# Kernel tuning notes

Measured on AMD Instinct MI355X. Metric: run time of the kernel, lower is better.

## Reference

```python
import jax, jax.numpy as jnp
import numpy as np

N = 4096
CIN = 128
COUT = 128
J = 2
SLOPE = 0.2        # LeakyReLU negative slope (GAT-style)
NEG = -9.0e15      # mask fill value from the source
ATT = J * COUT     # att_slice


def _leaky(v):
    return jnp.where(v >= 0, v, SLOPE * v)


def setup_inputs() -> dict:
    key = jax.random.key(0)
    ks = jax.random.split(key, 12)
    x = jax.random.normal(ks[0], (N, CIN), dtype=jnp.float32)

    def sparse_op(k):
        kv, km = jax.random.split(k)
        vals = jax.random.normal(kv, (N, N), dtype=jnp.float32)
        mask = jax.random.uniform(km, (N, N)) < 0.05
        return jnp.where(mask, vals, 0.0)

    Lu = sparse_op(ks[1])
    Ld = sparse_op(ks[2])
    P = jax.random.normal(ks[3], (N, N), dtype=jnp.float32) * 0.01  # harmonic projector

    s = 1.0 / np.sqrt(CIN)
    Wi_w = jax.random.uniform(ks[4], (J, CIN, COUT), minval=-s, maxval=s)
    Wi_b = jax.random.uniform(ks[5], (J, COUT), minval=-s, maxval=s)
    Ws_w = jax.random.uniform(ks[6], (J, CIN, COUT), minval=-s, maxval=s)
    Ws_b = jax.random.uniform(ks[7], (J, COUT), minval=-s, maxval=s)
    Wh_w = jax.random.uniform(ks[8], (CIN, COUT), minval=-s, maxval=s)
    Wh_b = jax.random.uniform(ks[9], (COUT,), minval=-s, maxval=s)
    att_irr = jax.random.normal(ks[10], (2 * ATT, 1), dtype=jnp.float32) * 0.1
    att_sol = jax.random.normal(ks[11], (2 * ATT, 1), dtype=jnp.float32) * 0.1
    return {"x": x, "Lu": Lu, "Ld": Ld, "P": P,
            "Wi_w": Wi_w, "Wi_b": Wi_b, "Ws_w": Ws_w, "Ws_b": Ws_b,
            "Wh_w": Wh_w, "Wh_b": Wh_b, "att_irr": att_irr, "att_sol": att_sol}


def reference(x, Lu, Ld, P, Wi_w, Wi_b, Ws_w, Ws_b, Wh_w, Wh_b, att_irr, att_sol):
    n = x.shape[0]
    # concat_j W_irr[j](x) -> [N, J*COUT] (j-major matches torch.cat along dim=1)
    x_irr = (jnp.einsum('nc,jco->njo', x, Wi_w) + Wi_b[None]).reshape(n, ATT)
    x_sol = (jnp.einsum('nc,jco->njo', x, Ws_w) + Ws_b[None]).reshape(n, ATT)

    # GAT-style scores: E[i,j] = leaky(s1[i] + s2[j])
    E_irr = _leaky(x_irr @ att_irr[:ATT] + (x_irr @ att_irr[ATT:]).T)
    E_sol = _leaky(x_sol @ att_sol[:ATT] + (x_sol @ att_sol[ATT:]).T)
    E_irr = jnp.where(Ld != 0, E_irr, NEG)
    E_sol = jnp.where(Lu != 0, E_sol, NEG)
    alpha_irr = jax.nn.softmax(E_irr, axis=1)  # dropout: eval mode -> identity
    alpha_sol = jax.nn.softmax(E_sol, axis=1)

    z = (alpha_irr @ x) @ Wi_w[0] + Wi_b[0] + (alpha_sol @ x) @ Ws_w[0] + Ws_b[0]
    for p in range(1, J):  # Laplacian-power aggregation
        alpha_irr = alpha_irr @ Ld
        alpha_sol = alpha_sol @ Lu
        z = z + (alpha_irr @ x) @ Wi_w[p] + Wi_b[p]
        z = z + (alpha_sol @ x) @ Ws_w[p] + Ws_b[p]
    z = z + (P @ x) @ Wh_w + Wh_b
    return z
```

## Files before the change

kernel.cpp:

```cpp
#include <hip/hip_runtime.h>

#define NN 4096
#define IDX_CAP 512
#define SEG_CAP 160
#define SLOPE 0.2f

typedef float f4_t __attribute__((ext_vector_type(4)));

#define V_OFF     0
#define C_OFF     512
#define BT_OFF    516
#define S_OFF     1024
#define HXI_OFF   32768
#define HXS_OFF   (HXI_OFF + NN*128)
#define UI_OFF    (HXS_OFF + NN*128)
#define US_OFF    (UI_OFF + NN*128)
#define XWH_OFF   (US_OFF + NN*128)
#define OI_OFF    (XWH_OFF + NN*128)
#define OS_OFF    (OI_OFF + NN*128)
#define ZP_OFF    (OS_OFF + NN*128)
#define WS_FLOATS (ZP_OFF + 8*NN*128)
#define IDX_BYTE_OFF ((size_t)WS_FLOATS * 4)
#define CNT_BYTE_OFF (IDX_BYTE_OFF + (size_t)2*NN*IDX_CAP*2)

__global__ __launch_bounds__(128) void k_prep(
    const float* __restrict__ Wi_w, const float* __restrict__ Wi_b,
    const float* __restrict__ Ws_w, const float* __restrict__ Ws_b,
    const float* __restrict__ Wh_b, const float* __restrict__ att_irr,
    const float* __restrict__ att_sol, float* __restrict__ ws) {
  const int t = threadIdx.x;
  float v1i = 0.f, v2i = 0.f, v1s = 0.f, v2s = 0.f;
  for (int j = 0; j < 2; ++j) {
    for (int o = 0; o < 128; ++o) {
      const float wi = Wi_w[j*16384 + t*128 + o];
      const float wv = Ws_w[j*16384 + t*128 + o];
      v1i += wi * att_irr[j*128 + o];
      v2i += wi * att_irr[256 + j*128 + o];
      v1s += wv * att_sol[j*128 + o];
      v2s += wv * att_sol[256 + j*128 + o];
    }
  }
  ws[V_OFF + t]       = v1i;
  ws[V_OFF + 128 + t] = v2i;
  ws[V_OFF + 256 + t] = v1s;
  ws[V_OFF + 384 + t] = v2s;
  ws[BT_OFF + t] = Wi_b[t] + Wi_b[128 + t] + Ws_b[t] + Ws_b[128 + t] + Wh_b[t];
  if (t < 4) {
    const float* bb = (t < 2) ? Wi_b : Ws_b;
    const float* aa = ((t < 2) ? att_irr : att_sol) + ((t & 1) ? 256 : 0);
    float c = 0.f;
    for (int k = 0; k < 256; ++k) c += bb[k] * aa[k];
    ws[C_OFF + t] = c;
  }
}

__global__ __launch_bounds__(256) void k_scores(const float* __restrict__ x,
                                                float* __restrict__ ws) {
  const int wave = threadIdx.x >> 6, lane = threadIdx.x & 63;
  const int row = blockIdx.x * 4 + wave;
  const float* v = ws + V_OFF;
  const float x0 = x[row*128 + lane];
  const float x1 = x[row*128 + 64 + lane];
  float p0 = x0 * v[lane]       + x1 * v[64 + lane];
  float p1 = x0 * v[128 + lane] + x1 * v[192 + lane];
  float p2 = x0 * v[256 + lane] + x1 * v[320 + lane];
  float p3 = x0 * v[384 + lane] + x1 * v[448 + lane];
  #pragma unroll
  for (int off = 32; off; off >>= 1) {
    p0 += __shfl_down(p0, off);
    p1 += __shfl_down(p1, off);
    p2 += __shfl_down(p2, off);
    p3 += __shfl_down(p3, off);
  }
  if (lane == 0) {
    ws[S_OFF + row]          = p0 + ws[C_OFF + 0];
    ws[S_OFF + NN + row]     = p1 + ws[C_OFF + 1];
    ws[S_OFF + 2*NN + row]   = p2 + ws[C_OFF + 2];
    ws[S_OFF + 3*NN + row]   = p3 + ws[C_OFF + 3];
  }
}

__global__ __launch_bounds__(256) void k_spmm_emit(
    const float* __restrict__ Ld, const float* __restrict__ Lu,
    const float* __restrict__ x, float* __restrict__ ws,
    unsigned short* __restrict__ idxbuf, int* __restrict__ cntbuf) {
  const int row = blockIdx.x & (NN - 1);
  const int br  = blockIdx.x >> 12;
  const float* __restrict__ Lrow = (br ? Lu : Ld) + (size_t)row * NN;
  float* __restrict__ Hx = ws + (br ? HXS_OFF : HXI_OFF);
  unsigned short* __restrict__ idxg = idxbuf + (size_t)(br*NN + row) * IDX_CAP;
  const float2* __restrict__ x2 = (const float2*)x;
  const int t = threadIdx.x;
  const int w = t >> 6, lane = t & 63;
  const unsigned long long lmask = (1ull << lane) - 1ull;

  __shared__ short jseg[4][SEG_CAP];
  __shared__ float vseg[4][SEG_CAP];
  __shared__ int   wcnt[4];
  __shared__ int   off[5];
  __shared__ short jl[IDX_CAP];
  __shared__ float vl[IDX_CAP];
  __shared__ float red[4][128];

  const f4_t* __restrict__ Lrow4 = (const f4_t*)Lrow;
  f4_t lv[4];
  #pragma unroll
  for (int i = 0; i < 4; ++i) lv[i] = __builtin_nontemporal_load(&Lrow4[i*256 + t]);

  int base = 0;
  #pragma unroll
  for (int i = 0; i < 4; ++i) {
    #pragma unroll
    for (int c = 0; c < 4; ++c) {
      const float v = lv[i][c];
      const unsigned long long bm = __ballot(v != 0.f);
      if (v != 0.f) {
        const int pos = base + (int)__popcll(bm & lmask);
        if (pos < SEG_CAP) {
          jseg[w][pos] = (short)((i*256 + t)*4 + c);
          vseg[w][pos] = v;
        }
      }
      base += (int)__popcll(bm);
    }
  }
  if (lane == 0) wcnt[w] = base;
  __syncthreads();
  if (t == 0) {
    int o = 0, ov = 0;
    #pragma unroll
    for (int s = 0; s < 4; ++s) { off[s] = o; ov |= (wcnt[s] > SEG_CAP); o += wcnt[s]; }
    off[4] = (ov || o > IDX_CAP) ? (IDX_CAP + 1) : o;
    cntbuf[br*NN + row] = off[4];
  }
  __syncthreads();
  const int m = off[4];

  if (m <= IDX_CAP) {
    const int o = off[w], c = wcnt[w];
    for (int k = lane; k < c; k += 64) {
      const short j = jseg[w][k];
      jl[o + k] = j;
      vl[o + k] = vseg[w][k];
      idxg[o + k] = (unsigned short)j;
    }
  }
  __syncthreads();

  float acc0 = 0.f, acc1 = 0.f;
  if (m <= IDX_CAP) {
    int p = w;
    for (; p + 28 < m; p += 32) {
      const int j0 = jl[p],    j1 = jl[p+4],  j2 = jl[p+8],  j3 = jl[p+12];
      const int j4 = jl[p+16], j5 = jl[p+20], j6 = jl[p+24], j7 = jl[p+28];
      const float v0 = vl[p],    v1 = vl[p+4],  v2 = vl[p+8],  v3 = vl[p+12];
      const float v4 = vl[p+16], v5 = vl[p+20], v6 = vl[p+24], v7 = vl[p+28];
      const float2 g0 = x2[j0*64 + lane];
      const float2 g1 = x2[j1*64 + lane];
      const float2 g2 = x2[j2*64 + lane];
      const float2 g3 = x2[j3*64 + lane];
      const float2 g4 = x2[j4*64 + lane];
      const float2 g5 = x2[j5*64 + lane];
      const float2 g6 = x2[j6*64 + lane];
      const float2 g7 = x2[j7*64 + lane];
      acc0 += v0*g0.x; acc1 += v0*g0.y;
      acc0 += v1*g1.x; acc1 += v1*g1.y;
      acc0 += v2*g2.x; acc1 += v2*g2.y;
      acc0 += v3*g3.x; acc1 += v3*g3.y;
      acc0 += v4*g4.x; acc1 += v4*g4.y;
      acc0 += v5*g5.x; acc1 += v5*g5.y;
      acc0 += v6*g6.x; acc1 += v6*g6.y;
      acc0 += v7*g7.x; acc1 += v7*g7.y;
    }
    for (; p < m; p += 4) {
      const int j = jl[p]; const float v = vl[p];
      const float2 g = x2[j*64 + lane];
      acc0 += v*g.x; acc1 += v*g.y;
    }
  } else {
    for (int j = w*1024; j < (w+1)*1024; ++j) {
      const float v = Lrow[j];
      if (v != 0.f) {
        const float2 g = x2[j*64 + lane];
        acc0 += v*g.x; acc1 += v*g.y;
      }
    }
  }
  red[w][lane*2]     = acc0;
  red[w][lane*2 + 1] = acc1;
  __syncthreads();
  if (t < 128)
    Hx[row*128 + t] = red[0][t] + red[1][t] + red[2][t] + red[3][t];
}

__global__ __launch_bounds__(256) void k_ugemm(
    const float* __restrict__ x, const float* __restrict__ Wi_w,
    const float* __restrict__ Ws_w, const float* __restrict__ Wh_w,
    float* __restrict__ ws) {
  const int rb = blockIdx.x;
  const int sel = blockIdx.y;
  const float* A[2]; const float* W[2]; int npass; float* out;
  if (sel == 0)      { A[0]=x; W[0]=Wi_w; A[1]=ws+HXI_OFF; W[1]=Wi_w+16384; npass=2; out=ws+UI_OFF; }
  else if (sel == 1) { A[0]=x; W[0]=Ws_w; A[1]=ws+HXS_OFF; W[1]=Ws_w+16384; npass=2; out=ws+US_OFF; }
  else               { A[0]=x; W[0]=Wh_w; A[1]=nullptr;    W[1]=nullptr;    npass=1; out=ws+XWH_OFF; }

  __shared__ __align__(16) float At[32][33];
  __shared__ __align__(16) float Wt[32][132];
  const int t = threadIdx.x;
  const int rg = t >> 4, cg = t & 15;
  const int r0 = rb * 32;
  float acc[2][8];
  #pragma unroll
  for (int i = 0; i < 2; ++i)
    #pragma unroll
    for (int j = 0; j < 8; ++j) acc[i][j] = 0.f;

  for (int ps = 0; ps < npass; ++ps) {
    const float* __restrict__ Ap = A[ps];
    const float* __restrict__ Wp = W[ps];
    for (int k0 = 0; k0 < 128; k0 += 32) {
      __syncthreads();
      {
        const int row = t >> 3, kq = t & 7;
        const float4 av = *(const float4*)&Ap[(r0 + row)*128 + k0 + kq*4];
        At[row][kq*4+0] = av.x; At[row][kq*4+1] = av.y;
        At[row][kq*4+2] = av.z; At[row][kq*4+3] = av.w;
      }
      #pragma unroll
      for (int l = 0; l < 4; ++l) {
        const int idx = t + l*256;
        const int kr = idx >> 5, c4 = idx & 31;
        const float4 wv = *(const float4*)&Wp[(k0 + kr)*128 + c4*4];
        Wt[kr][c4*4+0] = wv.x; Wt[kr][c4*4+1] = wv.y;
        Wt[kr][c4*4+2] = wv.z; Wt[kr][c4*4+3] = wv.w;
      }
      __syncthreads();
      #pragma unroll
      for (int k = 0; k < 32; ++k) {
        const float a0 = At[rg*2 + 0][k];
        const float a1 = At[rg*2 + 1][k];
        const float4 b0 = *(const float4*)&Wt[k][cg*8];
        const float4 b1 = *(const float4*)&Wt[k][cg*8 + 4];
        acc[0][0] += a0*b0.x; acc[0][1] += a0*b0.y; acc[0][2] += a0*b0.z; acc[0][3] += a0*b0.w;
        acc[0][4] += a0*b1.x; acc[0][5] += a0*b1.y; acc[0][6] += a0*b1.z; acc[0][7] += a0*b1.w;
        acc[1][0] += a1*b0.x; acc[1][1] += a1*b0.y; acc[1][2] += a1*b0.z; acc[1][3] += a1*b0.w;
        acc[1][4] += a1*b1.x; acc[1][5] += a1*b1.y; acc[1][6] += a1*b1.z; acc[1][7] += a1*b1.w;
      }
    }
  }
  #pragma unroll
  for (int i = 0; i < 2; ++i) {
    const int r = r0 + rg*2 + i;
    #pragma unroll
    for (int j = 0; j < 8; ++j) out[r*128 + cg*8 + j] = acc[i][j];
  }
}

__global__ __launch_bounds__(256) void k_pgemm(const float* __restrict__ P,
                                               const float* __restrict__ ws,
                                               float* __restrict__ zpart) {
  const int rbl = blockIdx.x;
  const int kz  = blockIdx.y;
  const float* __restrict__ Xw = ws + XWH_OFF;

  __shared__ __align__(16) float Pt[64][33];
  __shared__ __align__(16) float Xt[32][132];
  const int t = threadIdx.x;
  const int rg = t >> 4, cg = t & 15;
  const int r0 = rbl * 64;
  const int kbase = kz * 512;
  float acc[4][8];
  #pragma unroll
  for (int i = 0; i < 4; ++i)
    #pragma unroll
    for (int j = 0; j < 8; ++j) acc[i][j] = 0.f;

  for (int k0 = kbase; k0 < kbase + 512; k0 += 32) {
    __syncthreads();
    #pragma unroll
    for (int l = 0; l < 2; ++l) {
      const int idx = t + l*256;
      const int row = idx >> 3, kq = idx & 7;
      const float4 pv = *(const float4*)&P[(size_t)(r0 + row)*NN + k0 + kq*4];
      Pt[row][kq*4+0] = pv.x; Pt[row][kq*4+1] = pv.y;
      Pt[row][kq*4+2] = pv.z; Pt[row][kq*4+3] = pv.w;
    }
    #pragma unroll
    for (int l = 0; l < 4; ++l) {
      const int idx = t + l*256;
      const int kr = idx >> 5, c4 = idx & 31;
      const float4 xv = *(const float4*)&Xw[(k0 + kr)*128 + c4*4];
      Xt[kr][c4*4+0] = xv.x; Xt[kr][c4*4+1] = xv.y;
      Xt[kr][c4*4+2] = xv.z; Xt[kr][c4*4+3] = xv.w;
    }
    __syncthreads();
    #pragma unroll
    for (int k = 0; k < 32; ++k) {
      const float a0 = Pt[rg*4 + 0][k];
      const float a1 = Pt[rg*4 + 1][k];
      const float a2 = Pt[rg*4 + 2][k];
      const float a3 = Pt[rg*4 + 3][k];
      const float4 b0 = *(const float4*)&Xt[k][cg*8];
      const float4 b1 = *(const float4*)&Xt[k][cg*8 + 4];
      acc[0][0] += a0*b0.x; acc[0][1] += a0*b0.y; acc[0][2] += a0*b0.z; acc[0][3] += a0*b0.w;
      acc[0][4] += a0*b1.x; acc[0][5] += a0*b1.y; acc[0][6] += a0*b1.z; acc[0][7] += a0*b1.w;
      acc[1][0] += a1*b0.x; acc[1][1] += a1*b0.y; acc[1][2] += a1*b0.z; acc[1][3] += a1*b0.w;
      acc[1][4] += a1*b1.x; acc[1][5] += a1*b1.y; acc[1][6] += a1*b1.z; acc[1][7] += a1*b1.w;
      acc[2][0] += a2*b0.x; acc[2][1] += a2*b0.y; acc[2][2] += a2*b0.z; acc[2][3] += a2*b0.w;
      acc[2][4] += a2*b1.x; acc[2][5] += a2*b1.y; acc[2][6] += a2*b1.z; acc[2][7] += a2*b1.w;
      acc[3][0] += a3*b0.x; acc[3][1] += a3*b0.y; acc[3][2] += a3*b0.z; acc[3][3] += a3*b0.w;
      acc[3][4] += a3*b1.x; acc[3][5] += a3*b1.y; acc[3][6] += a3*b1.z; acc[3][7] += a3*b1.w;
    }
  }
  float* __restrict__ zp = zpart + (size_t)kz * NN * 128;
  #pragma unroll
  for (int i = 0; i < 4; ++i) {
    const int r = r0 + rg*4 + i;
    #pragma unroll
    for (int j = 0; j < 8; ++j) zp[r*128 + cg*8 + j] = acc[i][j];
  }
}

__global__ __launch_bounds__(256) void k_attn(
    const float* __restrict__ Ld, const float* __restrict__ Lu,
    float* __restrict__ ws, const unsigned short* __restrict__ idxbuf,
    const int* __restrict__ cntbuf) {
  const int row = blockIdx.x & (NN - 1);
  const int br  = blockIdx.x >> 12;
  const float* __restrict__ U = ws + (br ? US_OFF : UI_OFF);
  const float2* __restrict__ U2 = (const float2*)U;
  float* __restrict__ O = ws + (br ? OS_OFF : OI_OFF);
  const float s1 = ws[S_OFF + (br ? 2*NN : 0) + row];
  const float* __restrict__ s2a = ws + S_OFF + (br ? 3*NN : NN);
  const int cnt = cntbuf[br*NN + row];
  const int t = threadIdx.x;
  const int w = t >> 6, lane = t & 63;

  __shared__ int   jl[IDX_CAP];
  __shared__ float el[IDX_CAP];
  __shared__ float red[4][128];
  __shared__ float rsum[256];
  __shared__ float dsh[4];

  float acc0 = 0.f, acc1 = 0.f;
  if (cnt > 0 && cnt <= IDX_CAP) {
    const unsigned short* __restrict__ idx = idxbuf + (size_t)(br*NN + row) * IDX_CAP;
    float dpart = 0.f;
    for (int p = t; p < cnt; p += 256) {
      const int j = idx[p];
      const float sc = s1 + s2a[j];
      const float e = expf(sc >= 0.f ? sc : SLOPE * sc);
      jl[p] = j; el[p] = e; dpart += e;
    }
    rsum[t] = dpart;
    __syncthreads();
    if (t < 128) rsum[t] += rsum[t + 128];
    __syncthreads();
    if (t < 64) {
      float v = rsum[t] + rsum[t + 64];
      #pragma unroll
      for (int off = 32; off; off >>= 1) v += __shfl_down(v, off);
      if (t == 0) dsh[0] = v;
    }
    __syncthreads();
    const float den = dsh[0];
    int p = w;
    for (; p + 28 < cnt; p += 32) {
      const int j0 = jl[p],    j1 = jl[p+4],  j2 = jl[p+8],  j3 = jl[p+12];
      const int j4 = jl[p+16], j5 = jl[p+20], j6 = jl[p+24], j7 = jl[p+28];
      const float e0 = el[p],    e1 = el[p+4],  e2 = el[p+8],  e3 = el[p+12];
      const float e4 = el[p+16], e5 = el[p+20], e6 = el[p+24], e7 = el[p+28];
      const float2 g0 = U2[j0*64 + lane];
      const float2 g1 = U2[j1*64 + lane];
      const float2 g2 = U2[j2*64 + lane];
      const float2 g3 = U2[j3*64 + lane];
      const float2 g4 = U2[j4*64 + lane];
      const float2 g5 = U2[j5*64 + lane];
      const float2 g6 = U2[j6*64 + lane];
      const float2 g7 = U2[j7*64 + lane];
      acc0 += e0*g0.x; acc1 += e0*g0.y;
      acc0 += e1*g1.x; acc1 += e1*g1.y;
      acc0 += e2*g2.x; acc1 += e2*g2.y;
      acc0 += e3*g3.x; acc1 += e3*g3.y;
      acc0 += e4*g4.x; acc1 += e4*g4.y;
      acc0 += e5*g5.x; acc1 += e5*g5.y;
      acc0 += e6*g6.x; acc1 += e6*g6.y;
      acc0 += e7*g7.x; acc1 += e7*g7.y;
    }
    for (; p < cnt; p += 4) {
      const int j = jl[p]; const float e = el[p];
      const float2 g = U2[j*64 + lane];
      acc0 += e*g.x; acc1 += e*g.y;
    }
    red[w][lane*2]     = acc0;
    red[w][lane*2 + 1] = acc1;
    __syncthreads();
    if (t < 128)
      O[row*128 + t] = (red[0][t] + red[1][t] + red[2][t] + red[3][t]) / den;
  } else if (cnt == 0) {
    for (int j = w*1024; j < (w+1)*1024; ++j) {
      const float2 g = U2[j*64 + lane];
      acc0 += g.x; acc1 += g.y;
    }
    red[w][lane*2]     = acc0;
    red[w][lane*2 + 1] = acc1;
    __syncthreads();
    if (t < 128)
      O[row*128 + t] = (red[0][t] + red[1][t] + red[2][t] + red[3][t]) * (1.f / NN);
  } else {
    const float* __restrict__ Lrow = (br ? Lu : Ld) + (size_t)row * NN;
    float dp = 0.f;
    for (int j = w*1024; j < (w+1)*1024; ++j) {
      const float v = Lrow[j];
      if (v != 0.f) {
        const float sc = s1 + s2a[j];
        const float e = expf(sc >= 0.f ? sc : SLOPE * sc);
        const float2 g = U2[j*64 + lane];
        acc0 += e*g.x; acc1 += e*g.y;
        dp += e;
      }
    }
    if (lane == 0) dsh[w] = dp;
    red[w][lane*2]     = acc0;
    red[w][lane*2 + 1] = acc1;
    __syncthreads();
    const float den = dsh[0] + dsh[1] + dsh[2] + dsh[3];
    if (t < 128)
      O[row*128 + t] = (red[0][t] + red[1][t] + red[2][t] + red[3][t]) / den;
  }
}

__global__ __launch_bounds__(256) void k_combine(const float* __restrict__ ws,
                                                 float* __restrict__ z) {
  const int i = blockIdx.x * 256 + threadIdx.x;
  const int col = i & 127;
  float acc = ws[BT_OFF + col] + ws[OI_OFF + i] + ws[OS_OFF + i];
  #pragma unroll
  for (int kz = 0; kz < 8; ++kz) acc += ws[ZP_OFF + kz*NN*128 + i];
  z[i] = acc;
}

extern "C" void kernel_launch(void* const* d_in, const int* in_sizes, int n_in,
                              void* d_out, int out_size, void* d_ws, size_t ws_size,
                              hipStream_t stream) {
  const float* x       = (const float*)d_in[0];
  const float* Lu      = (const float*)d_in[1];
  const float* Ld      = (const float*)d_in[2];
  const float* P       = (const float*)d_in[3];
  const float* Wi_w    = (const float*)d_in[4];
  const float* Wi_b    = (const float*)d_in[5];
  const float* Ws_w    = (const float*)d_in[6];
  const float* Ws_b    = (const float*)d_in[7];
  const float* Wh_w    = (const float*)d_in[8];
  const float* Wh_b    = (const float*)d_in[9];
  const float* att_irr = (const float*)d_in[10];
  const float* att_sol = (const float*)d_in[11];
  float* z  = (float*)d_out;
  float* ws = (float*)d_ws;
  unsigned short* idxbuf = (unsigned short*)((char*)d_ws + IDX_BYTE_OFF);
  int*            cntbuf = (int*)((char*)d_ws + CNT_BYTE_OFF);

  k_prep<<<1, 128, 0, stream>>>(Wi_w, Wi_b, Ws_w, Ws_b, Wh_b, att_irr, att_sol, ws);
  k_scores<<<1024, 256, 0, stream>>>(x, ws);
  k_spmm_emit<<<2 * NN, 256, 0, stream>>>(Ld, Lu, x, ws, idxbuf, cntbuf);
  {
    dim3 g(128, 3);
    k_ugemm<<<g, 256, 0, stream>>>(x, Wi_w, Ws_w, Wh_w, ws);
  }
  {
    dim3 g(64, 8);
    k_pgemm<<<g, 256, 0, stream>>>(P, ws, ws + ZP_OFF);
  }
  k_attn<<<2 * NN, 256, 0, stream>>>(Ld, Lu, ws, idxbuf, cntbuf);
  k_combine<<<NN * 128 / 256, 256, 0, stream>>>(ws, z);
}
```

Before: 399.0 us.

## Restructure gathers to float4, swizzle LDS tiles, split pgemm columns, interleave branch rows

The x@Wh GEMM moves into a merged pre-pass kernel alongside the score computation. The sparse gather loops in spmm_emit and attn now use 16-byte loads, with half-waves covering alternate nonzeros and a cross-half shuffle reduction. Block-to-row mapping interleaves the Ld and Lu branches, and LDS weight tiles get a padded swizzle to avoid bank conflicts. The P GEMM is split into two column halves to double the block count, and the launch order is changed. The combined edits aim to raise gather bandwidth and occupancy, at the cost of more index arithmetic and smaller per-block tiles in pgemm.

```diff
diff --git a/kernel.cpp b/kernel.cpp
--- a/kernel.cpp
+++ b/kernel.cpp
@@ -23,6 +23,11 @@
 #define IDX_BYTE_OFF ((size_t)WS_FLOATS * 4)
 #define CNT_BYTE_OFF (IDX_BYTE_OFF + (size_t)2*NN*IDX_CAP*2)
 
+#define XI(c)   ((c) + (((c) >> 5) << 2))
+
+#define MAP_BR(bid)   (((bid) >> 2) & 1)
+#define MAP_ROW(bid)  ((((bid) >> 3) << 2) | ((bid) & 3))
+
 __global__ __launch_bounds__(128) void k_prep(
     const float* __restrict__ Wi_w, const float* __restrict__ Wi_b,
     const float* __restrict__ Ws_w, const float* __restrict__ Ws_b,
@@ -54,29 +59,80 @@
   }
 }
 
-__global__ __launch_bounds__(256) void k_scores(const float* __restrict__ x,
-                                                float* __restrict__ ws) {
-  const int wave = threadIdx.x >> 6, lane = threadIdx.x & 63;
-  const int row = blockIdx.x * 4 + wave;
-  const float* v = ws + V_OFF;
-  const float x0 = x[row*128 + lane];
-  const float x1 = x[row*128 + 64 + lane];
-  float p0 = x0 * v[lane]       + x1 * v[64 + lane];
-  float p1 = x0 * v[128 + lane] + x1 * v[192 + lane];
-  float p2 = x0 * v[256 + lane] + x1 * v[320 + lane];
-  float p3 = x0 * v[384 + lane] + x1 * v[448 + lane];
-  #pragma unroll
-  for (int off = 32; off; off >>= 1) {
-    p0 += __shfl_down(p0, off);
-    p1 += __shfl_down(p1, off);
-    p2 += __shfl_down(p2, off);
-    p3 += __shfl_down(p3, off);
-  }
-  if (lane == 0) {
-    ws[S_OFF + row]          = p0 + ws[C_OFF + 0];
-    ws[S_OFF + NN + row]     = p1 + ws[C_OFF + 1];
-    ws[S_OFF + 2*NN + row]   = p2 + ws[C_OFF + 2];
-    ws[S_OFF + 3*NN + row]   = p3 + ws[C_OFF + 3];
+__global__ __launch_bounds__(256) void k_pre2(
+    const float* __restrict__ x, const float* __restrict__ Wh_w,
+    float* __restrict__ ws) {
+  __shared__ __align__(16) float At[32][33];
+  __shared__ __align__(16) float Wt[32][144];
+  const int t = threadIdx.x;
+
+  if (blockIdx.x < 128) {
+    const int rb = blockIdx.x;
+    float* out = ws + XWH_OFF;
+    const int rg = t >> 4, cg = t & 15;
+    const int r0 = rb * 32;
+    float acc[2][8];
+    #pragma unroll
+    for (int i = 0; i < 2; ++i)
+      #pragma unroll
+      for (int j = 0; j < 8; ++j) acc[i][j] = 0.f;
+    for (int k0 = 0; k0 < 128; k0 += 32) {
+      __syncthreads();
+      {
+        const int row = t >> 3, kq = t & 7;
+        const float4 av = *(const float4*)&x[(r0 + row)*128 + k0 + kq*4];
+        At[row][kq*4+0] = av.x; At[row][kq*4+1] = av.y;
+        At[row][kq*4+2] = av.z; At[row][kq*4+3] = av.w;
+      }
+      #pragma unroll
+      for (int l = 0; l < 4; ++l) {
+        const int idx = t + l*256;
+        const int kr = idx >> 5, c4 = idx & 31;
+        const float4 wv = *(const float4*)&Wh_w[(k0 + kr)*128 + c4*4];
+        *(float4*)&Wt[kr][XI(c4*4)] = wv;
+      }
+      __syncthreads();
+      #pragma unroll
+      for (int k = 0; k < 32; ++k) {
+        const float a0 = At[rg*2 + 0][k];
+        const float a1 = At[rg*2 + 1][k];
+        const float4 b0 = *(const float4*)&Wt[k][XI(cg*8)];
+        const float4 b1 = *(const float4*)&Wt[k][XI(cg*8 + 4)];
+        acc[0][0] += a0*b0.x; acc[0][1] += a0*b0.y; acc[0][2] += a0*b0.z; acc[0][3] += a0*b0.w;
+        acc[0][4] += a0*b1.x; acc[0][5] += a0*b1.y; acc[0][6] += a0*b1.z; acc[0][7] += a0*b1.w;
+        acc[1][0] += a1*b0.x; acc[1][1] += a1*b0.y; acc[1][2] += a1*b0.z; acc[1][3] += a1*b0.w;
+        acc[1][4] += a1*b1.x; acc[1][5] += a1*b1.y; acc[1][6] += a1*b1.z; acc[1][7] += a1*b1.w;
+      }
+    }
+    #pragma unroll
+    for (int i = 0; i < 2; ++i) {
+      const int r = r0 + rg*2 + i;
+      #pragma unroll
+      for (int j = 0; j < 8; ++j) out[r*128 + cg*8 + j] = acc[i][j];
+    }
+  } else {
+    const int wave = t >> 6, lane = t & 63;
+    const int row = (blockIdx.x - 128) * 4 + wave;
+    const float* v = ws + V_OFF;
+    const float x0 = x[row*128 + lane];
+    const float x1 = x[row*128 + 64 + lane];
+    float p0 = x0 * v[lane]       + x1 * v[64 + lane];
+    float p1 = x0 * v[128 + lane] + x1 * v[192 + lane];
+    float p2 = x0 * v[256 + lane] + x1 * v[320 + lane];
+    float p3 = x0 * v[384 + lane] + x1 * v[448 + lane];
+    #pragma unroll
+    for (int off = 32; off; off >>= 1) {
+      p0 += __shfl_down(p0, off);
+      p1 += __shfl_down(p1, off);
+      p2 += __shfl_down(p2, off);
+      p3 += __shfl_down(p3, off);
+    }
+    if (lane == 0) {
+      ws[S_OFF + row]          = p0 + ws[C_OFF + 0];
+      ws[S_OFF + NN + row]     = p1 + ws[C_OFF + 1];
+      ws[S_OFF + 2*NN + row]   = p2 + ws[C_OFF + 2];
+      ws[S_OFF + 3*NN + row]   = p3 + ws[C_OFF + 3];
+    }
   }
 }
 
@@ -84,12 +140,12 @@
     const float* __restrict__ Ld, const float* __restrict__ Lu,
     const float* __restrict__ x, float* __restrict__ ws,
     unsigned short* __restrict__ idxbuf, int* __restrict__ cntbuf) {
-  const int row = blockIdx.x & (NN - 1);
-  const int br  = blockIdx.x >> 12;
+  const int bid = blockIdx.x;
+  const int br  = MAP_BR(bid);
+  const int row = MAP_ROW(bid);
   const float* __restrict__ Lrow = (br ? Lu : Ld) + (size_t)row * NN;
   float* __restrict__ Hx = ws + (br ? HXS_OFF : HXI_OFF);
   unsigned short* __restrict__ idxg = idxbuf + (size_t)(br*NN + row) * IDX_CAP;
-  const float2* __restrict__ x2 = (const float2*)x;
   const int t = threadIdx.x;
   const int w = t >> 6, lane = t & 63;
   const unsigned long long lmask = (1ull << lane) - 1ull;
@@ -147,37 +203,35 @@
   }
   __syncthreads();
 
-  float acc0 = 0.f, acc1 = 0.f;
   if (m <= IDX_CAP) {
+    const f4_t* __restrict__ x4 = (const f4_t*)x;
+    const int li = lane & 31, half = lane >> 5;
+    f4_t acc = {0.f, 0.f, 0.f, 0.f};
     int p = w;
-    for (; p + 28 < m; p += 32) {
-      const int j0 = jl[p],    j1 = jl[p+4],  j2 = jl[p+8],  j3 = jl[p+12];
-      const int j4 = jl[p+16], j5 = jl[p+20], j6 = jl[p+24], j7 = jl[p+28];
-      const float v0 = vl[p],    v1 = vl[p+4],  v2 = vl[p+8],  v3 = vl[p+12];
-      const float v4 = vl[p+16], v5 = vl[p+20], v6 = vl[p+24], v7 = vl[p+28];
-      const float2 g0 = x2[j0*64 + lane];
-      const float2 g1 = x2[j1*64 + lane];
-      const float2 g2 = x2[j2*64 + lane];
-      const float2 g3 = x2[j3*64 + lane];
-      const float2 g4 = x2[j4*64 + lane];
-      const float2 g5 = x2[j5*64 + lane];
-      const float2 g6 = x2[j6*64 + lane];
-      const float2 g7 = x2[j7*64 + lane];
-      acc0 += v0*g0.x; acc1 += v0*g0.y;
-      acc0 += v1*g1.x; acc1 += v1*g1.y;
-      acc0 += v2*g2.x; acc1 += v2*g2.y;
-      acc0 += v3*g3.x; acc1 += v3*g3.y;
-      acc0 += v4*g4.x; acc1 += v4*g4.y;
-      acc0 += v5*g5.x; acc1 += v5*g5.y;
-      acc0 += v6*g6.x; acc1 += v6*g6.y;
-      acc0 += v7*g7.x; acc1 += v7*g7.y;
-    }
-    for (; p < m; p += 4) {
-      const int j = jl[p]; const float v = vl[p];
-      const float2 g = x2[j*64 + lane];
-      acc0 += v*g.x; acc1 += v*g.y;
+    for (; 2*(p + 12) + 1 < m; p += 16) {
+      const int q0 = 2*p + half, q1 = 2*(p+4) + half,
+                q2 = 2*(p+8) + half, q3 = 2*(p+12) + half;
+      const int j0 = jl[q0], j1 = jl[q1], j2 = jl[q2], j3 = jl[q3];
+      const float v0 = vl[q0], v1 = vl[q1], v2 = vl[q2], v3 = vl[q3];
+      const f4_t g0 = x4[j0*32 + li];
+      const f4_t g1 = x4[j1*32 + li];
+      const f4_t g2 = x4[j2*32 + li];
+      const f4_t g3 = x4[j3*32 + li];
+      acc += v0*g0; acc += v1*g1; acc += v2*g2; acc += v3*g3;
+    }
+    for (; 2*p < m; p += 4) {
+      const int q = 2*p + half;
+      if (q < m) acc += vl[q] * x4[jl[q]*32 + li];
+    }
+    #pragma unroll
+    for (int c = 0; c < 4; ++c) acc[c] += __shfl_xor(acc[c], 32);
+    if (half == 0) {
+      red[w][li*4+0] = acc[0]; red[w][li*4+1] = acc[1];
+      red[w][li*4+2] = acc[2]; red[w][li*4+3] = acc[3];
     }
   } else {
+    const float2* __restrict__ x2 = (const float2*)x;
+    float acc0 = 0.f, acc1 = 0.f;
     for (int j = w*1024; j < (w+1)*1024; ++j) {
       const float v = Lrow[j];
       if (v != 0.f) {
@@ -185,9 +239,9 @@
         acc0 += v*g.x; acc1 += v*g.y;
       }
     }
-  }
-  red[w][lane*2]     = acc0;
-  red[w][lane*2 + 1] = acc1;
+    red[w][lane*2]     = acc0;
+    red[w][lane*2 + 1] = acc1;
+  }
   __syncthreads();
   if (t < 128)
     Hx[row*128 + t] = red[0][t] + red[1][t] + red[2][t] + red[3][t];
@@ -195,17 +249,15 @@
 
 __global__ __launch_bounds__(256) void k_ugemm(
     const float* __restrict__ x, const float* __restrict__ Wi_w,
-    const float* __restrict__ Ws_w, const float* __restrict__ Wh_w,
-    float* __restrict__ ws) {
+    const float* __restrict__ Ws_w, float* __restrict__ ws) {
   const int rb = blockIdx.x;
   const int sel = blockIdx.y;
-  const float* A[2]; const float* W[2]; int npass; float* out;
-  if (sel == 0)      { A[0]=x; W[0]=Wi_w; A[1]=ws+HXI_OFF; W[1]=Wi_w+16384; npass=2; out=ws+UI_OFF; }
-  else if (sel == 1) { A[0]=x; W[0]=Ws_w; A[1]=ws+HXS_OFF; W[1]=Ws_w+16384; npass=2; out=ws+US_OFF; }
-  else               { A[0]=x; W[0]=Wh_w; A[1]=nullptr;    W[1]=nullptr;    npass=1; out=ws+XWH_OFF; }
+  const float* A[2]; const float* W[2]; float* out;
+  if (sel == 0) { A[0]=x; W[0]=Wi_w; A[1]=ws+HXI_OFF; W[1]=Wi_w+16384; out=ws+UI_OFF; }
+  else          { A[0]=x; W[0]=Ws_w; A[1]=ws+HXS_OFF; W[1]=Ws_w+16384; out=ws+US_OFF; }
 
   __shared__ __align__(16) float At[32][33];
-  __shared__ __align__(16) float Wt[32][132];
+  __shared__ __align__(16) float Wt[32][144];
   const int t = threadIdx.x;
   const int rg = t >> 4, cg = t & 15;
   const int r0 = rb * 32;
@@ -215,7 +267,7 @@
     #pragma unroll
     for (int j = 0; j < 8; ++j) acc[i][j] = 0.f;
 
-  for (int ps = 0; ps < npass; ++ps) {
+  for (int ps = 0; ps < 2; ++ps) {
     const float* __restrict__ Ap = A[ps];
     const float* __restrict__ Wp = W[ps];
     for (int k0 = 0; k0 < 128; k0 += 32) {
@@ -231,16 +283,15 @@
         const int idx = t + l*256;
         const int kr = idx >> 5, c4 = idx & 31;
         const float4 wv = *(const float4*)&Wp[(k0 + kr)*128 + c4*4];
-        Wt[kr][c4*4+0] = wv.x; Wt[kr][c4*4+1] = wv.y;
-        Wt[kr][c4*4+2] = wv.z; Wt[kr][c4*4+3] = wv.w;
+        *(float4*)&Wt[kr][XI(c4*4)] = wv;
       }
       __syncthreads();
       #pragma unroll
       for (int k = 0; k < 32; ++k) {
         const float a0 = At[rg*2 + 0][k];
         const float a1 = At[rg*2 + 1][k];
-        const float4 b0 = *(const float4*)&Wt[k][cg*8];
-        const float4 b1 = *(const float4*)&Wt[k][cg*8 + 4];
+        const float4 b0 = *(const float4*)&Wt[k][XI(cg*8)];
+        const float4 b1 = *(const float4*)&Wt[k][XI(cg*8 + 4)];
         acc[0][0] += a0*b0.x; acc[0][1] += a0*b0.y; acc[0][2] += a0*b0.z; acc[0][3] += a0*b0.w;
         acc[0][4] += a0*b1.x; acc[0][5] += a0*b1.y; acc[0][6] += a0*b1.z; acc[0][7] += a0*b1.w;
         acc[1][0] += a1*b0.x; acc[1][1] += a1*b0.y; acc[1][2] += a1*b0.z; acc[1][3] += a1*b0.w;
@@ -256,79 +307,14 @@
   }
 }
 
-__global__ __launch_bounds__(256) void k_pgemm(const float* __restrict__ P,
-                                               const float* __restrict__ ws,
-                                               float* __restrict__ zpart) {
-  const int rbl = blockIdx.x;
-  const int kz  = blockIdx.y;
-  const float* __restrict__ Xw = ws + XWH_OFF;
-
-  __shared__ __align__(16) float Pt[64][33];
-  __shared__ __align__(16) float Xt[32][132];
-  const int t = threadIdx.x;
-  const int rg = t >> 4, cg = t & 15;
-  const int r0 = rbl * 64;
-  const int kbase = kz * 512;
-  float acc[4][8];
-  #pragma unroll
-  for (int i = 0; i < 4; ++i)
-    #pragma unroll
-    for (int j = 0; j < 8; ++j) acc[i][j] = 0.f;
-
-  for (int k0 = kbase; k0 < kbase + 512; k0 += 32) {
-    __syncthreads();
-    #pragma unroll
-    for (int l = 0; l < 2; ++l) {
-      const int idx = t + l*256;
-      const int row = idx >> 3, kq = idx & 7;
-      const float4 pv = *(const float4*)&P[(size_t)(r0 + row)*NN + k0 + kq*4];
-      Pt[row][kq*4+0] = pv.x; Pt[row][kq*4+1] = pv.y;
-      Pt[row][kq*4+2] = pv.z; Pt[row][kq*4+3] = pv.w;
-    }
-    #pragma unroll
-    for (int l = 0; l < 4; ++l) {
-      const int idx = t + l*256;
-      const int kr = idx >> 5, c4 = idx & 31;
-      const float4 xv = *(const float4*)&Xw[(k0 + kr)*128 + c4*4];
-      Xt[kr][c4*4+0] = xv.x; Xt[kr][c4*4+1] = xv.y;
-      Xt[kr][c4*4+2] = xv.z; Xt[kr][c4*4+3] = xv.w;
-    }
-    __syncthreads();
-    #pragma unroll
-    for (int k = 0; k < 32; ++k) {
-      const float a0 = Pt[rg*4 + 0][k];
-      const float a1 = Pt[rg*4 + 1][k];
-      const float a2 = Pt[rg*4 + 2][k];
-      const float a3 = Pt[rg*4 + 3][k];
-      const float4 b0 = *(const float4*)&Xt[k][cg*8];
-      const float4 b1 = *(const float4*)&Xt[k][cg*8 + 4];
-      acc[0][0] += a0*b0.x; acc[0][1] += a0*b0.y; acc[0][2] += a0*b0.z; acc[0][3] += a0*b0.w;
-      acc[0][4] += a0*b1.x; acc[0][5] += a0*b1.y; acc[0][6] += a0*b1.z; acc[0][7] += a0*b1.w;
-      acc[1][0] += a1*b0.x; acc[1][1] += a1*b0.y; acc[1][2] += a1*b0.z; acc[1][3] += a1*b0.w;
-      acc[1][4] += a1*b1.x; acc[1][5] += a1*b1.y; acc[1][6] += a1*b1.z; acc[1][7] += a1*b1.w;
-      acc[2][0] += a2*b0.x; acc[2][1] += a2*b0.y; acc[2][2] += a2*b0.z; acc[2][3] += a2*b0.w;
-      acc[2][4] += a2*b1.x; acc[2][5] += a2*b1.y; acc[2][6] += a2*b1.z; acc[2][7] += a2*b1.w;
-      acc[3][0] += a3*b0.x; acc[3][1] += a3*b0.y; acc[3][2] += a3*b0.z; acc[3][3] += a3*b0.w;
-      acc[3][4] += a3*b1.x; acc[3][5] += a3*b1.y; acc[3][6] += a3*b1.z; acc[3][7] += a3*b1.w;
-    }
-  }
-  float* __restrict__ zp = zpart + (size_t)kz * NN * 128;
-  #pragma unroll
-  for (int i = 0; i < 4; ++i) {
-    const int r = r0 + rg*4 + i;
-    #pragma unroll
-    for (int j = 0; j < 8; ++j) zp[r*128 + cg*8 + j] = acc[i][j];
-  }
-}
-
 __global__ __launch_bounds__(256) void k_attn(
     const float* __restrict__ Ld, const float* __restrict__ Lu,
     float* __restrict__ ws, const unsigned short* __restrict__ idxbuf,
     const int* __restrict__ cntbuf) {
-  const int row = blockIdx.x & (NN - 1);
-  const int br  = blockIdx.x >> 12;
+  const int bid = blockIdx.x;
+  const int br  = MAP_BR(bid);
+  const int row = MAP_ROW(bid);
   const float* __restrict__ U = ws + (br ? US_OFF : UI_OFF);
-  const float2* __restrict__ U2 = (const float2*)U;
   float* __restrict__ O = ws + (br ? OS_OFF : OI_OFF);
   const float s1 = ws[S_OFF + (br ? 2*NN : 0) + row];
   const float* __restrict__ s2a = ws + S_OFF + (br ? 3*NN : NN);
@@ -342,7 +328,6 @@
   __shared__ float rsum[256];
   __shared__ float dsh[4];
 
-  float acc0 = 0.f, acc1 = 0.f;
   if (cnt > 0 && cnt <= IDX_CAP) {
     const unsigned short* __restrict__ idx = idxbuf + (size_t)(br*NN + row) * IDX_CAP;
     float dpart = 0.f;
@@ -364,40 +349,37 @@
     }
     __syncthreads();
     const float den = dsh[0];
+    const f4_t* __restrict__ U4 = (const f4_t*)U;
+    const int li = lane & 31, half = lane >> 5;
+    f4_t acc = {0.f, 0.f, 0.f, 0.f};
     int p = w;
-    for (; p + 28 < cnt; p += 32) {
-      const int j0 = jl[p],    j1 = jl[p+4],  j2 = jl[p+8],  j3 = jl[p+12];
-      const int j4 = jl[p+16], j5 = jl[p+20], j6 = jl[p+24], j7 = jl[p+28];
-      const float e0 = el[p],    e1 = el[p+4],  e2 = el[p+8],  e3 = el[p+12];
-      const float e4 = el[p+16], e5 = el[p+20], e6 = el[p+24], e7 = el[p+28];
-      const float2 g0 = U2[j0*64 + lane];
-      const float2 g1 = U2[j1*64 + lane];
-      const float2 g2 = U2[j2*64 + lane];
-      const float2 g3 = U2[j3*64 + lane];
-      const float2 g4 = U2[j4*64 + lane];
-      const float2 g5 = U2[j5*64 + lane];
-      const float2 g6 = U2[j6*64 + lane];
-      const float2 g7 = U2[j7*64 + lane];
-      acc0 += e0*g0.x; acc1 += e0*g0.y;
-      acc0 += e1*g1.x; acc1 += e1*g1.y;
-      acc0 += e2*g2.x; acc1 += e2*g2.y;
-      acc0 += e3*g3.x; acc1 += e3*g3.y;
-      acc0 += e4*g4.x; acc1 += e4*g4.y;
-      acc0 += e5*g5.x; acc1 += e5*g5.y;
-      acc0 += e6*g6.x; acc1 += e6*g6.y;
-      acc0 += e7*g7.x; acc1 += e7*g7.y;
-    }
-    for (; p < cnt; p += 4) {
-      const int j = jl[p]; const float e = el[p];
-      const float2 g = U2[j*64 + lane];
-      acc0 += e*g.x; acc1 += e*g.y;
-    }
-    red[w][lane*2]     = acc0;
-    red[w][lane*2 + 1] = acc1;
+    for (; 2*(p + 12) + 1 < cnt; p += 16) {
+      const int q0 = 2*p + half, q1 = 2*(p+4) + half,
+                q2 = 2*(p+8) + half, q3 = 2*(p+12) + half;
+      const int j0 = jl[q0], j1 = jl[q1], j2 = jl[q2], j3 = jl[q3];
+      const float e0 = el[q0], e1 = el[q1], e2 = el[q2], e3 = el[q3];
+      const f4_t g0 = U4[j0*32 + li];
+      const f4_t g1 = U4[j1*32 + li];
+      const f4_t g2 = U4[j2*32 + li];
+      const f4_t g3 = U4[j3*32 + li];
+      acc += e0*g0; acc += e1*g1; acc += e2*g2; acc += e3*g3;
+    }
+    for (; 2*p < cnt; p += 4) {
+      const int q = 2*p + half;
+      if (q < cnt) acc += el[q] * U4[jl[q]*32 + li];
+    }
+    #pragma unroll
+    for (int c = 0; c < 4; ++c) acc[c] += __shfl_xor(acc[c], 32);
+    if (half == 0) {
+      red[w][li*4+0] = acc[0]; red[w][li*4+1] = acc[1];
+      red[w][li*4+2] = acc[2]; red[w][li*4+3] = acc[3];
+    }
     __syncthreads();
     if (t < 128)
       O[row*128 + t] = (red[0][t] + red[1][t] + red[2][t] + red[3][t]) / den;
   } else if (cnt == 0) {
+    const float2* __restrict__ U2 = (const float2*)U;
+    float acc0 = 0.f, acc1 = 0.f;
     for (int j = w*1024; j < (w+1)*1024; ++j) {
       const float2 g = U2[j*64 + lane];
       acc0 += g.x; acc1 += g.y;
@@ -409,7 +391,8 @@
       O[row*128 + t] = (red[0][t] + red[1][t] + red[2][t] + red[3][t]) * (1.f / NN);
   } else {
     const float* __restrict__ Lrow = (br ? Lu : Ld) + (size_t)row * NN;
-    float dp = 0.f;
+    const float2* __restrict__ U2 = (const float2*)U;
+    float acc0 = 0.f, acc1 = 0.f, dp = 0.f;
     for (int j = w*1024; j < (w+1)*1024; ++j) {
       const float v = Lrow[j];
       if (v != 0.f) {
@@ -427,6 +410,69 @@
     const float den = dsh[0] + dsh[1] + dsh[2] + dsh[3];
     if (t < 128)
       O[row*128 + t] = (red[0][t] + red[1][t] + red[2][t] + red[3][t]) / den;
+  }
+}
+
+__global__ __launch_bounds__(256) void k_pgemm(const float* __restrict__ P,
+                                               const float* __restrict__ ws,
+                                               float* __restrict__ zpart) {
+  const int rbl = blockIdx.x & 63;
+  const int nb  = blockIdx.x >> 6;
+  const int kz  = blockIdx.y;
+  const float* __restrict__ Xw = ws + XWH_OFF;
+
+  __shared__ __align__(16) float Pt[64][33];
+  __shared__ __align__(16) float Xt[32][72];
+  const int t = threadIdx.x;
+  const int rg = t >> 4, cg = t & 15;
+  const int r0 = rbl * 64;
+  const int c0 = nb * 64;
+  const int kbase = kz * 512;
+  float acc[4][4];
+  #pragma unroll
+  for (int i = 0; i < 4; ++i)
+    #pragma unroll
+    for (int j = 0; j < 4; ++j) acc[i][j] = 0.f;
+
+  for (int k0 = kbase; k0 < kbase + 512; k0 += 32) {
+    __syncthreads();
+    #pragma unroll
+    for (int l = 0; l < 2; ++l) {
+      const int idx = t + l*256;
+      const int row = idx >> 3, kq = idx & 7;
+      const float4 pv = *(const float4*)&P[(size_t)(r0 + row)*NN + k0 + kq*4];
+      Pt[row][kq*4+0] = pv.x; Pt[row][kq*4+1] = pv.y;
+      Pt[row][kq*4+2] = pv.z; Pt[row][kq*4+3] = pv.w;
+    }
+    {
+      #pragma unroll
+      for (int l = 0; l < 2; ++l) {
+        const int idx = t + l*256;
+        const int kr = idx >> 4, c4 = idx & 15;
+        const float4 xv = *(const float4*)&Xw[(k0 + kr)*128 + c0 + c4*4];
+        *(float4*)&Xt[kr][XI(c4*4)] = xv;
+      }
+    }
+    __syncthreads();
+    #pragma unroll
+    for (int k = 0; k < 32; ++k) {
+      const float a0 = Pt[rg*4 + 0][k];
+      const float a1 = Pt[rg*4 + 1][k];
+      const float a2 = Pt[rg*4 + 2][k];
+      const float a3 = Pt[rg*4 + 3][k];
+      const float4 b = *(const float4*)&Xt[k][XI(cg*4)];
+      acc[0][0] += a0*b.x; acc[0][1] += a0*b.y; acc[0][2] += a0*b.z; acc[0][3] += a0*b.w;
+      acc[1][0] += a1*b.x; acc[1][1] += a1*b.y; acc[1][2] += a1*b.z; acc[1][3] += a1*b.w;
+      acc[2][0] += a2*b.x; acc[2][1] += a2*b.y; acc[2][2] += a2*b.z; acc[2][3] += a2*b.w;
+      acc[3][0] += a3*b.x; acc[3][1] += a3*b.y; acc[3][2] += a3*b.z; acc[3][3] += a3*b.w;
+    }
+  }
+  float* __restrict__ zp = zpart + (size_t)kz * NN * 128;
+  #pragma unroll
+  for (int i = 0; i < 4; ++i) {
+    const int r = r0 + rg*4 + i;
+    #pragma unroll
+    for (int j = 0; j < 4; ++j) zp[r*128 + c0 + cg*4 + j] = acc[i][j];
   }
 }
 
@@ -459,18 +505,19 @@
   float* ws = (float*)d_ws;
   unsigned short* idxbuf = (unsigned short*)((char*)d_ws + IDX_BYTE_OFF);
   int*            cntbuf = (int*)((char*)d_ws + CNT_BYTE_OFF);
+  float*          zpart  = ws + ZP_OFF;
 
   k_prep<<<1, 128, 0, stream>>>(Wi_w, Wi_b, Ws_w, Ws_b, Wh_b, att_irr, att_sol, ws);
-  k_scores<<<1024, 256, 0, stream>>>(x, ws);
+  k_pre2<<<1152, 256, 0, stream>>>(x, Wh_w, ws);
   k_spmm_emit<<<2 * NN, 256, 0, stream>>>(Ld, Lu, x, ws, idxbuf, cntbuf);
   {
-    dim3 g(128, 3);
-    k_ugemm<<<g, 256, 0, stream>>>(x, Wi_w, Ws_w, Wh_w, ws);
-  }
+    dim3 g(128, 2);
+    k_ugemm<<<g, 256, 0, stream>>>(x, Wi_w, Ws_w, ws);
+  }
+  k_attn<<<2 * NN, 256, 0, stream>>>(Ld, Lu, ws, idxbuf, cntbuf);
   {
-    dim3 g(64, 8);
-    k_pgemm<<<g, 256, 0, stream>>>(P, ws, ws + ZP_OFF);
-  }
-  k_attn<<<2 * NN, 256, 0, stream>>>(Ld, Lu, ws, idxbuf, cntbuf);
+    dim3 g(128, 8);
+    k_pgemm<<<g, 256, 0, stream>>>(P, ws, zpart);
+  }
   k_combine<<<NN * 128 / 256, 256, 0, stream>>>(ws, z);
 }
```

Result: faster. 373.5 us (-6.4%).
